# Kernel tuning notes

Measured on AMD Instinct MI355X. Metric: run time of the kernel, lower is better.

Reference implementation:

```python
import jax, jax.numpy as jnp
import numpy as np

N = 1048576          # number of sample points
C = 32               # feature_dim per plane
PAIRS = ((0, 1), (0, 2), (1, 2))  # itertools.combinations(range(3), 2)


def setup_inputs() -> dict:
    key = jax.random.key(0)
    k0, k1, k2, k3 = jax.random.split(key, 4)
    # grid_sample coords must lie in [-1, 1]
    x = jax.random.uniform(k0, (N, 3), jnp.float32, -1.0, 1.0)
    # torch.nn.init.uniform_ default is U[0, 1)
    planes_128 = jax.random.uniform(k1, (3, C, 128, 128), jnp.float32)
    planes_256 = jax.random.uniform(k2, (3, C, 256, 256), jnp.float32)
    planes_512 = jax.random.uniform(k3, (3, C, 512, 512), jnp.float32)
    return {"x": x, "planes_128": planes_128, "planes_256": planes_256,
            "planes_512": planes_512}


def _bilinear_sample(plane, coords):
    """plane: (C, H, W); coords: (N, 2) in [-1,1], last dim = (x, y).
    Matches torch grid_sample(mode='bilinear', align_corners=True).
    Returns (N, C)."""
    _, H, W = plane.shape
    gx, gy = coords[:, 0], coords[:, 1]
    ix = (gx + 1.0) * 0.5 * (W - 1)   # x indexes width
    iy = (gy + 1.0) * 0.5 * (H - 1)   # y indexes height
    x0f = jnp.clip(jnp.floor(ix), 0.0, W - 1)
    y0f = jnp.clip(jnp.floor(iy), 0.0, H - 1)
    wx = ix - x0f
    wy = iy - y0f
    x0 = x0f.astype(jnp.int32)
    y0 = y0f.astype(jnp.int32)
    x1 = jnp.minimum(x0 + 1, W - 1)
    y1 = jnp.minimum(y0 + 1, H - 1)
    v00 = plane[:, y0, x0]  # (C, N)
    v01 = plane[:, y0, x1]
    v10 = plane[:, y1, x0]
    v11 = plane[:, y1, x1]
    out = (v00 * (1 - wx) * (1 - wy) + v01 * wx * (1 - wy)
           + v10 * (1 - wx) * wy + v11 * wx * wy)  # (C, N)
    return out.T  # (N, C)


def reference(x, planes_128, planes_256, planes_512):
    # coords[p] = x[:, (i, j)] for pair p -> grid (x=dim i, y=dim j)
    coords = jnp.stack([x[:, jnp.array(p)] for p in PAIRS])  # (3, N, 2)
    feats = []
    for planes in (planes_128, planes_256, planes_512):
        sampled = jax.vmap(_bilinear_sample)(planes, coords)  # (3, N, C)
        feats.append(jnp.prod(sampled, axis=0))               # (N, C)
    return jnp.concatenate(feats, axis=-1)  # (N, 96); dropout(p=0) is identity
```

## Files before the change

### kernel.cpp

```cpp
#include <hip/hip_runtime.h>
#include <hip/hip_fp16.h>


constexpr int kN = 1048576;
constexpr int kC = 32;
constexpr int kCells = 32 * 32 * 32;

typedef float f32x4 __attribute__((ext_vector_type(4)));
typedef short s16x4 __attribute__((ext_vector_type(4)));

__global__ __launch_bounds__(1024) void kp_transpose_h(const float* __restrict__ in,
                                                       __half* __restrict__ out, int R) {
    __shared__ float tile[32][33];
    const int tx = threadIdx.x, ty = threadIdx.y;
    const int x0 = blockIdx.x * 32;
    const int y  = blockIdx.y;
    const int p  = blockIdx.z;
    tile[ty][tx] = in[(((size_t)p * kC + ty) * R + y) * R + x0 + tx];
    __syncthreads();
    out[(((size_t)p * R + y) * R + x0 + ty) * kC + tx] = __float2half_rn(tile[tx][ty]);
}

__device__ __forceinline__ unsigned cell_key(float x, float y, float z) {
    int cx = min(max((int)((x + 1.f) * 16.f), 0), 31);
    int cy = min(max((int)((y + 1.f) * 16.f), 0), 31);
    int cz = min(max((int)((z + 1.f) * 16.f), 0), 31);
    unsigned m = 0;
#pragma unroll
    for (int b = 0; b < 5; ++b) {
        m |= ((unsigned)((cx >> b) & 1)) << (3 * b);
        m |= ((unsigned)((cy >> b) & 1)) << (3 * b + 1);
        m |= ((unsigned)((cz >> b) & 1)) << (3 * b + 2);
    }
    return m;
}

__global__ __launch_bounds__(256) void kp_zero(unsigned* __restrict__ p, int n) {
    int i = blockIdx.x * 256 + threadIdx.x;
    if (i < n) p[i] = 0u;
}

__global__ __launch_bounds__(256) void kp_hist(const float* __restrict__ xs,
                                               unsigned* __restrict__ hist) {
    int n = blockIdx.x * 256 + threadIdx.x;
    float x = xs[n * 3 + 0], y = xs[n * 3 + 1], z = xs[n * 3 + 2];
    atomicAdd(&hist[cell_key(x, y, z)], 1u);
}

__global__ __launch_bounds__(1024) void kp_scan(const unsigned* __restrict__ hist,
                                                unsigned* __restrict__ cursor) {
    __shared__ unsigned sums[1024];
    const int t = threadIdx.x;
    const int per = kCells / 1024;
    unsigned local[32];
    unsigned s = 0;
    const int base = t * per;
#pragma unroll
    for (int i = 0; i < per; ++i) { local[i] = hist[base + i]; s += local[i]; }
    sums[t] = s;
    __syncthreads();
    for (int off = 1; off < 1024; off <<= 1) {
        unsigned v = (t >= off) ? sums[t - off] : 0u;
        __syncthreads();
        sums[t] += v;
        __syncthreads();
    }
    unsigned run = (t == 0) ? 0u : sums[t - 1];
#pragma unroll
    for (int i = 0; i < per; ++i) { cursor[base + i] = run; run += local[i]; }
}

__global__ __launch_bounds__(256) void kp_scatter(const float* __restrict__ xs,
                                                  unsigned* __restrict__ cursor,
                                                  f32x4* __restrict__ sorted) {
    int n = blockIdx.x * 256 + threadIdx.x;
    float x = xs[n * 3 + 0], y = xs[n * 3 + 1], z = xs[n * 3 + 2];
    unsigned pos = atomicAdd(&cursor[cell_key(x, y, z)], 1u);
    f32x4 v = {x, y, z, __uint_as_float((unsigned)n)};
    sorted[pos] = v;
}

__device__ __forceinline__ void load4h(const __half* __restrict__ p, float* v) {
    union { s16x4 s; __half2 h[2]; } u;
    u.s = *reinterpret_cast<const s16x4*>(p);
    float2 f01 = __half22float2(u.h[0]);
    float2 f23 = __half22float2(u.h[1]);
    v[0] = f01.x; v[1] = f01.y; v[2] = f23.x; v[3] = f23.y;
}

template<int R>
__device__ __forceinline__ void sample_res(const __half* __restrict__ planes, int c4,
                                           const float* gx, const float* gy, float* f) {
    const float fr = (float)(R - 1);
    f[0] = f[1] = f[2] = f[3] = 1.f;
#pragma unroll
    for (int p = 0; p < 3; ++p) {
        float ix = (gx[p] + 1.f) * 0.5f * fr;
        float iy = (gy[p] + 1.f) * 0.5f * fr;
        float x0f = fminf(fmaxf(floorf(ix), 0.f), fr);
        float y0f = fminf(fmaxf(floorf(iy), 0.f), fr);
        float wx = ix - x0f, wy = iy - y0f;
        int xi0 = (int)x0f, yi0 = (int)y0f;
        int xi1 = min(xi0 + 1, R - 1), yi1 = min(yi0 + 1, R - 1);
        const __half* pl = planes + (size_t)p * R * R * kC + c4;
        float v00[4], v01[4], v10[4], v11[4];
        load4h(pl + (yi0 * R + xi0) * kC, v00);
        load4h(pl + (yi0 * R + xi1) * kC, v01);
        load4h(pl + (yi1 * R + xi0) * kC, v10);
        load4h(pl + (yi1 * R + xi1) * kC, v11);
        float w00 = (1.f - wx) * (1.f - wy), w01 = wx * (1.f - wy);
        float w10 = (1.f - wx) * wy,         w11 = wx * wy;
#pragma unroll
        for (int j = 0; j < 4; ++j)
            f[j] *= w00 * v00[j] + w01 * v01[j] + w10 * v10[j] + w11 * v11[j];
    }
}

__global__ __launch_bounds__(256) void kp_sample_sorted(const f32x4* __restrict__ pts,
                                                        const __half* __restrict__ t128,
                                                        const __half* __restrict__ t256,
                                                        const __half* __restrict__ t512,
                                                        float* __restrict__ out) {
    const int nwg = (kN * 8) / 256;
    int bid = blockIdx.x;
    bid = (bid & 7) * (nwg / 8) + (bid >> 3);
    const int li = threadIdx.x;
    const int n  = bid * 32 + (li >> 3);
    const int c4 = (li & 7) << 2;
    f32x4 pt = pts[n];
    const float a = pt.x, b = pt.y, d = pt.z;
    const unsigned oi = __float_as_uint(pt.w);
    const float gx[3] = {a, a, b};
    const float gy[3] = {b, d, d};
    float* o = out + (size_t)oi * 96 + c4;
    float f[4];
    sample_res<128>(t128, c4, gx, gy, f);
    __builtin_nontemporal_store(f32x4{f[0], f[1], f[2], f[3]}, (f32x4*)(o + 0));
    sample_res<256>(t256, c4, gx, gy, f);
    __builtin_nontemporal_store(f32x4{f[0], f[1], f[2], f[3]}, (f32x4*)(o + 32));
    sample_res<512>(t512, c4, gx, gy, f);
    __builtin_nontemporal_store(f32x4{f[0], f[1], f[2], f[3]}, (f32x4*)(o + 64));
}

template<int R>
__global__ __launch_bounds__(256) void kp_sample_h(const float* __restrict__ xs,
                                                   const __half* __restrict__ planes,
                                                   float* __restrict__ out, int rbase) {
    const int t = blockIdx.x * 256 + (int)threadIdx.x;
    const int n  = t >> 3;
    const int c4 = (t & 7) << 2;
    const float a = xs[n * 3 + 0], b = xs[n * 3 + 1], d = xs[n * 3 + 2];
    const float gx[3] = {a, a, b};
    const float gy[3] = {b, d, d};
    float f[4];
    sample_res<R>(planes, c4, gx, gy, f);
    __builtin_nontemporal_store(f32x4{f[0], f[1], f[2], f[3]},
                                (f32x4*)(out + (size_t)n * 96 + rbase + c4));
}

__global__ __launch_bounds__(256) void kp_sample_f32(const float* __restrict__ xs,
                                                     const float* __restrict__ p128,
                                                     const float* __restrict__ p256,
                                                     const float* __restrict__ p512,
                                                     float* __restrict__ out) {
    const int t = blockIdx.x * 256 + (int)threadIdx.x;
    const int n = t >> 5;
    const int c = t & 31;
    const float a = xs[n * 3 + 0], b = xs[n * 3 + 1], d = xs[n * 3 + 2];
    const float gxs[3] = {a, a, b};
    const float gys[3] = {b, d, d};
    const float* planes[3] = {p128, p256, p512};
    const int Rs[3] = {128, 256, 512};
    float* o = out + (size_t)n * 96;
#pragma unroll
    for (int r = 0; r < 3; ++r) {
        const int R = Rs[r];
        const float fr = (float)(R - 1);
        float f = 1.0f;
#pragma unroll
        for (int p = 0; p < 3; ++p) {
            float ix = (gxs[p] + 1.f) * 0.5f * fr;
            float iy = (gys[p] + 1.f) * 0.5f * fr;
            float x0f = fminf(fmaxf(floorf(ix), 0.f), fr);
            float y0f = fminf(fmaxf(floorf(iy), 0.f), fr);
            float wx = ix - x0f, wy = iy - y0f;
            int xi0 = (int)x0f, yi0 = (int)y0f;
            int xi1 = min(xi0 + 1, R - 1), yi1 = min(yi0 + 1, R - 1);
            const float* pc = planes[r] + ((size_t)p * kC + c) * R * R;
            float v00 = pc[yi0 * R + xi0], v01 = pc[yi0 * R + xi1];
            float v10 = pc[yi1 * R + xi0], v11 = pc[yi1 * R + xi1];
            f *= v00 * (1.f - wx) * (1.f - wy) + v01 * wx * (1.f - wy)
               + v10 * (1.f - wx) * wy + v11 * wx * wy;
        }
        __builtin_nontemporal_store(f, o + r * 32 + c);
    }
}

extern "C" void kernel_launch(void* const* d_in, const int* in_sizes, int n_in,
                              void* d_out, int out_size, void* d_ws, size_t ws_size,
                              hipStream_t stream) {
    const float* xs   = (const float*)d_in[0];
    const float* p128 = (const float*)d_in[1];
    const float* p256 = (const float*)d_in[2];
    const float* p512 = (const float*)d_in[3];
    float* out = (float*)d_out;

    const size_t n128 = (size_t)3 * 128 * 128 * kC;
    const size_t n256 = (size_t)3 * 256 * 256 * kC;
    const size_t n512 = (size_t)3 * 512 * 512 * kC;
    const size_t planes_b = (n128 + n256 + n512) * sizeof(__half);
    const size_t sorted_b = (size_t)kN * 16;
    const size_t hist_b   = (size_t)kCells * 4;
    const size_t need_sorted = sorted_b + planes_b + 2 * hist_b + 256;
    const size_t need_plain  = planes_b;

    dim3 tblk(32, 32);
    const int nblk8 = (kN * 8) / 256;

    if (ws_size >= need_sorted) {
        f32x4* sorted = (f32x4*)d_ws;
        __half* t128 = (__half*)((char*)d_ws + sorted_b);
        __half* t256 = t128 + n128;
        __half* t512 = t256 + n256;
        unsigned* hist   = (unsigned*)((char*)d_ws + sorted_b + planes_b);
        unsigned* cursor = hist + kCells;

        kp_transpose_h<<<dim3(128 / 32, 128, 3), tblk, 0, stream>>>(p128, t128, 128);
        kp_transpose_h<<<dim3(256 / 32, 256, 3), tblk, 0, stream>>>(p256, t256, 256);
        kp_transpose_h<<<dim3(512 / 32, 512, 3), tblk, 0, stream>>>(p512, t512, 512);
        kp_zero<<<(kCells + 255) / 256, 256, 0, stream>>>(hist, kCells);
        kp_hist<<<kN / 256, 256, 0, stream>>>(xs, hist);
        kp_scan<<<1, 1024, 0, stream>>>(hist, cursor);
        kp_scatter<<<kN / 256, 256, 0, stream>>>(xs, cursor, sorted);
        kp_sample_sorted<<<nblk8, 256, 0, stream>>>(sorted, t128, t256, t512, out);
    } else if (ws_size >= need_plain) {
        __half* t128 = (__half*)d_ws;
        __half* t256 = t128 + n128;
        __half* t512 = t256 + n256;
        kp_transpose_h<<<dim3(128 / 32, 128, 3), tblk, 0, stream>>>(p128, t128, 128);
        kp_transpose_h<<<dim3(256 / 32, 256, 3), tblk, 0, stream>>>(p256, t256, 256);
        kp_transpose_h<<<dim3(512 / 32, 512, 3), tblk, 0, stream>>>(p512, t512, 512);
        kp_sample_h<128><<<nblk8, 256, 0, stream>>>(xs, t128, out, 0);
        kp_sample_h<256><<<nblk8, 256, 0, stream>>>(xs, t256, out, 32);
        kp_sample_h<512><<<nblk8, 256, 0, stream>>>(xs, t512, out, 64);
    } else {
        kp_sample_f32<<<(kN * 32) / 256, 256, 0, stream>>>(xs, p128, p256, p512, out);
    }
}
```

Baseline: 341.4 us.

## Store each texel paired with its right neighbor to halve gather loads

The preprocessing transpose now writes each channel as a half2 holding the texel value and its x+1 neighbor, with the last column clamped. The sampler can then fetch both horizontal taps with one 16-byte load per row, cutting four gathers per plane to two, and it uses lerp-form interpolation. The cost is a duplicated plane layout with twice the bytes to write during the transpose and twice the cache footprint during sampling. The scatter store is also made nontemporal, and the plain-workspace fallback path is removed, so any workspace smaller than the sorted path's need now drops straight to the fp32 kernel.

```diff
diff --git a/kernel.cpp b/kernel.cpp
--- a/kernel.cpp
+++ b/kernel.cpp
@@ -7,18 +7,23 @@
 constexpr int kCells = 32 * 32 * 32;
 
 typedef float f32x4 __attribute__((ext_vector_type(4)));
-typedef short s16x4 __attribute__((ext_vector_type(4)));
-
-__global__ __launch_bounds__(1024) void kp_transpose_h(const float* __restrict__ in,
-                                                       __half* __restrict__ out, int R) {
+typedef short s16x8 __attribute__((ext_vector_type(8)));
+
+__global__ __launch_bounds__(1024) void kp_transpose_dup(const float* __restrict__ in,
+                                                         __half2* __restrict__ out, int R) {
     __shared__ float tile[32][33];
     const int tx = threadIdx.x, ty = threadIdx.y;
     const int x0 = blockIdx.x * 32;
     const int y  = blockIdx.y;
     const int p  = blockIdx.z;
     tile[ty][tx] = in[(((size_t)p * kC + ty) * R + y) * R + x0 + tx];
+    if (ty == 0) {
+        int xl = min(x0 + 32, R - 1);
+        tile[tx][32] = in[(((size_t)p * kC + tx) * R + y) * R + xl];
+    }
     __syncthreads();
-    out[(((size_t)p * R + y) * R + x0 + ty) * kC + tx] = __float2half_rn(tile[tx][ty]);
+    __half2 v = __floats2half2_rn(tile[tx][ty], tile[tx][ty + 1]);
+    out[(((size_t)p * R + y) * R + x0 + ty) * 32 + tx] = v;
 }
 
 __device__ __forceinline__ unsigned cell_key(float x, float y, float z) {
@@ -77,20 +82,12 @@
     float x = xs[n * 3 + 0], y = xs[n * 3 + 1], z = xs[n * 3 + 2];
     unsigned pos = atomicAdd(&cursor[cell_key(x, y, z)], 1u);
     f32x4 v = {x, y, z, __uint_as_float((unsigned)n)};
-    sorted[pos] = v;
-}
-
-__device__ __forceinline__ void load4h(const __half* __restrict__ p, float* v) {
-    union { s16x4 s; __half2 h[2]; } u;
-    u.s = *reinterpret_cast<const s16x4*>(p);
-    float2 f01 = __half22float2(u.h[0]);
-    float2 f23 = __half22float2(u.h[1]);
-    v[0] = f01.x; v[1] = f01.y; v[2] = f23.x; v[3] = f23.y;
+    __builtin_nontemporal_store(v, &sorted[pos]);
 }
 
 template<int R>
-__device__ __forceinline__ void sample_res(const __half* __restrict__ planes, int c4,
-                                           const float* gx, const float* gy, float* f) {
+__device__ __forceinline__ void sample_res_dup(const __half* __restrict__ planes, int c4,
+                                               const float* gx, const float* gy, float* f) {
     const float fr = (float)(R - 1);
     f[0] = f[1] = f[2] = f[3] = 1.f;
 #pragma unroll
@@ -101,18 +98,19 @@
         float y0f = fminf(fmaxf(floorf(iy), 0.f), fr);
         float wx = ix - x0f, wy = iy - y0f;
         int xi0 = (int)x0f, yi0 = (int)y0f;
-        int xi1 = min(xi0 + 1, R - 1), yi1 = min(yi0 + 1, R - 1);
-        const __half* pl = planes + (size_t)p * R * R * kC + c4;
-        float v00[4], v01[4], v10[4], v11[4];
-        load4h(pl + (yi0 * R + xi0) * kC, v00);
-        load4h(pl + (yi0 * R + xi1) * kC, v01);
-        load4h(pl + (yi1 * R + xi0) * kC, v10);
-        load4h(pl + (yi1 * R + xi1) * kC, v11);
-        float w00 = (1.f - wx) * (1.f - wy), w01 = wx * (1.f - wy);
-        float w10 = (1.f - wx) * wy,         w11 = wx * wy;
-#pragma unroll
-        for (int j = 0; j < 4; ++j)
-            f[j] *= w00 * v00[j] + w01 * v01[j] + w10 * v10[j] + w11 * v11[j];
+        int yi1 = min(yi0 + 1, R - 1);
+        const __half* pl = planes + (size_t)p * R * R * 64 + (size_t)c4 * 2;
+        union U { s16x8 s; __half2 h[4]; } r0, r1;
+        r0.s = *reinterpret_cast<const s16x8*>(pl + ((size_t)yi0 * R + xi0) * 64);
+        r1.s = *reinterpret_cast<const s16x8*>(pl + ((size_t)yi1 * R + xi0) * 64);
+#pragma unroll
+        for (int j = 0; j < 4; ++j) {
+            float2 q0 = __half22float2(r0.h[j]);
+            float2 q1 = __half22float2(r1.h[j]);
+            float vx0 = q0.x + wx * (q0.y - q0.x);
+            float vx1 = q1.x + wx * (q1.y - q1.x);
+            f[j] *= vx0 + wy * (vx1 - vx0);
+        }
     }
 }
 
@@ -134,28 +132,12 @@
     const float gy[3] = {b, d, d};
     float* o = out + (size_t)oi * 96 + c4;
     float f[4];
-    sample_res<128>(t128, c4, gx, gy, f);
-    __builtin_nontemporal_store(f32x4{f[0], f[1], f[2], f[3]}, (f32x4*)(o + 0));
-    sample_res<256>(t256, c4, gx, gy, f);
+    sample_res_dup<128>(t128, c4, gx, gy, f);
+    __builtin_nontemporal_store(f32x4{f[0], f[1], f[2], f[3]}, (f32x4*)o);
+    sample_res_dup<256>(t256, c4, gx, gy, f);
     __builtin_nontemporal_store(f32x4{f[0], f[1], f[2], f[3]}, (f32x4*)(o + 32));
-    sample_res<512>(t512, c4, gx, gy, f);
+    sample_res_dup<512>(t512, c4, gx, gy, f);
     __builtin_nontemporal_store(f32x4{f[0], f[1], f[2], f[3]}, (f32x4*)(o + 64));
-}
-
-template<int R>
-__global__ __launch_bounds__(256) void kp_sample_h(const float* __restrict__ xs,
-                                                   const __half* __restrict__ planes,
-                                                   float* __restrict__ out, int rbase) {
-    const int t = blockIdx.x * 256 + (int)threadIdx.x;
-    const int n  = t >> 3;
-    const int c4 = (t & 7) << 2;
-    const float a = xs[n * 3 + 0], b = xs[n * 3 + 1], d = xs[n * 3 + 2];
-    const float gx[3] = {a, a, b};
-    const float gy[3] = {b, d, d};
-    float f[4];
-    sample_res<R>(planes, c4, gx, gy, f);
-    __builtin_nontemporal_store(f32x4{f[0], f[1], f[2], f[3]},
-                                (f32x4*)(out + (size_t)n * 96 + rbase + c4));
 }
 
 __global__ __launch_bounds__(256) void kp_sample_f32(const float* __restrict__ xs,
@@ -205,19 +187,18 @@
     const float* p512 = (const float*)d_in[3];
     float* out = (float*)d_out;
 
-    const size_t n128 = (size_t)3 * 128 * 128 * kC;
-    const size_t n256 = (size_t)3 * 256 * 256 * kC;
-    const size_t n512 = (size_t)3 * 512 * 512 * kC;
+    const size_t n128 = (size_t)3 * 128 * 128 * 64;
+    const size_t n256 = (size_t)3 * 256 * 256 * 64;
+    const size_t n512 = (size_t)3 * 512 * 512 * 64;
     const size_t planes_b = (n128 + n256 + n512) * sizeof(__half);
     const size_t sorted_b = (size_t)kN * 16;
     const size_t hist_b   = (size_t)kCells * 4;
-    const size_t need_sorted = sorted_b + planes_b + 2 * hist_b + 256;
-    const size_t need_plain  = planes_b;
+    const size_t need = sorted_b + planes_b + 2 * hist_b + 256;
 
     dim3 tblk(32, 32);
     const int nblk8 = (kN * 8) / 256;
 
-    if (ws_size >= need_sorted) {
+    if (ws_size >= need) {
         f32x4* sorted = (f32x4*)d_ws;
         __half* t128 = (__half*)((char*)d_ws + sorted_b);
         __half* t256 = t128 + n128;
@@ -225,24 +206,14 @@
         unsigned* hist   = (unsigned*)((char*)d_ws + sorted_b + planes_b);
         unsigned* cursor = hist + kCells;
 
-        kp_transpose_h<<<dim3(128 / 32, 128, 3), tblk, 0, stream>>>(p128, t128, 128);
-        kp_transpose_h<<<dim3(256 / 32, 256, 3), tblk, 0, stream>>>(p256, t256, 256);
-        kp_transpose_h<<<dim3(512 / 32, 512, 3), tblk, 0, stream>>>(p512, t512, 512);
+        kp_transpose_dup<<<dim3(128 / 32, 128, 3), tblk, 0, stream>>>(p128, (__half2*)t128, 128);
+        kp_transpose_dup<<<dim3(256 / 32, 256, 3), tblk, 0, stream>>>(p256, (__half2*)t256, 256);
+        kp_transpose_dup<<<dim3(512 / 32, 512, 3), tblk, 0, stream>>>(p512, (__half2*)t512, 512);
         kp_zero<<<(kCells + 255) / 256, 256, 0, stream>>>(hist, kCells);
         kp_hist<<<kN / 256, 256, 0, stream>>>(xs, hist);
         kp_scan<<<1, 1024, 0, stream>>>(hist, cursor);
         kp_scatter<<<kN / 256, 256, 0, stream>>>(xs, cursor, sorted);
         kp_sample_sorted<<<nblk8, 256, 0, stream>>>(sorted, t128, t256, t512, out);
-    } else if (ws_size >= need_plain) {
-        __half* t128 = (__half*)d_ws;
-        __half* t256 = t128 + n128;
-        __half* t512 = t256 + n256;
-        kp_transpose_h<<<dim3(128 / 32, 128, 3), tblk, 0, stream>>>(p128, t128, 128);
-        kp_transpose_h<<<dim3(256 / 32, 256, 3), tblk, 0, stream>>>(p256, t256, 256);
-        kp_transpose_h<<<dim3(512 / 32, 512, 3), tblk, 0, stream>>>(p512, t512, 512);
-        kp_sample_h<128><<<nblk8, 256, 0, stream>>>(xs, t128, out, 0);
-        kp_sample_h<256><<<nblk8, 256, 0, stream>>>(xs, t256, out, 32);
-        kp_sample_h<512><<<nblk8, 256, 0, stream>>>(xs, t512, out, 64);
     } else {
         kp_sample_f32<<<(kN * 32) / 256, 256, 0, stream>>>(xs, p128, p256, p512, out);
     }
```

After: 428.7 us. +25.6%, slower.
